# Optimization experiments

Hardware: AMD Instinct MI355X
Metric: run time of the kernel (lower is better)

The kernel has to match this reference:

```python
import jax, jax.numpy as jnp
import numpy as np

INPUT_DIM = 1024
HIDDEN_DIM = 512
SEQ_LEN = 512


def setup_inputs() -> dict:
    key = jax.random.key(0)
    ks = jax.random.split(key, 7)
    s = 1.0 / np.sqrt(INPUT_DIM)
    s2 = 1.0 / np.sqrt(HIDDEN_DIM)
    return {
        "vectors": jax.random.normal(ks[0], (1, SEQ_LEN, INPUT_DIM), dtype=jnp.float32),
        "W_h": jax.random.uniform(ks[1], (HIDDEN_DIM, INPUT_DIM), jnp.float32, -s, s),
        "b_h": jax.random.uniform(ks[2], (HIDDEN_DIM,), jnp.float32, -s, s),
        "W_m": jax.random.uniform(ks[3], (HIDDEN_DIM, INPUT_DIM), jnp.float32, -s, s),
        "b_m": jax.random.uniform(ks[4], (HIDDEN_DIM,), jnp.float32, -s, s),
        "w2": jax.random.uniform(ks[5], (HIDDEN_DIM,), jnp.float32, -s2, s2),
        "b2": jax.random.uniform(ks[6], (), jnp.float32, -s2, s2),
    }


def reference(vectors, W_h, b_h, W_m, b_m, w2, b2):
    # vectors: [1, S, D] -> squeeze leading batch dim (matches torch .squeeze(0))
    x = vectors[0]  # [S, D]
    # Two batched GEMMs replacing the per-token Python loop
    H = x @ W_h.T + b_h  # [S, Hd] head representations
    M = x @ W_m.T + b_m  # [S, Hd] modifier representations
    # Pairwise broadcast add + tanh + dot with layer_2 weights -> [S, S] scores
    pair = jnp.tanh(H[:, None, :] + M[None, :, :])  # [S, S, Hd]
    scores = jnp.einsum('hmd,d->hm', pair, w2) + b2
    return scores
```

## Files before the change

### kernel.cpp

```cpp
#include <hip/hip_runtime.h>

#define C2 2.8853900817779268f
#define DIN 1024
#define HD 512

__device__ __forceinline__ float rcp_fast(float x){ return __builtin_amdgcn_rcpf(x); }
__device__ __forceinline__ float exp2_fast(float x){ return __builtin_amdgcn_exp2f(x); }
__device__ __forceinline__ float comp4(const float4& v, int i){
    return i==0 ? v.x : i==1 ? v.y : i==2 ? v.z : v.w;
}

__global__ __launch_bounds__(256, 4) void gemm_kernel(
    const float* __restrict__ x, const float* __restrict__ Wh,
    const float* __restrict__ Wm, float* __restrict__ P)
{
    int mat = blockIdx.z >> 3, slice = blockIdx.z & 7;
    const float* W = mat ? Wm : Wh;
    int s0 = blockIdx.y * 64, j0 = blockIdx.x * 64;
    int k0base = slice * 128;
    __shared__ float Xs[64 * 32];
    __shared__ float Ws[64 * 32];
    int tid = threadIdx.x;
    int tx = tid & 15, ty = tid >> 4;
    int lrow = tid >> 3, lq = tid & 7;

    const float* xp = x + (size_t)(s0 + lrow) * DIN + k0base + lq * 4;
    const float* wp = W + (size_t)(j0 + lrow) * DIN + k0base + lq * 4;

    auto sidx = [](int row, int q){ return row * 32 + ((q ^ ((row >> 2) & 7)) << 2); };

    float4 xr0, xr1, wr0, wr1;
    auto load_chunk = [&](int c){
        int off = c * 32;
        xr0 = *(const float4*)(xp + off);
        xr1 = *(const float4*)(xp + off + 32 * DIN);
        wr0 = *(const float4*)(wp + off);
        wr1 = *(const float4*)(wp + off + 32 * DIN);
    };
    auto store_chunk = [&](){
        *(float4*)&Xs[sidx(lrow, lq)]      = xr0;
        *(float4*)&Xs[sidx(lrow + 32, lq)] = xr1;
        *(float4*)&Ws[sidx(lrow, lq)]      = wr0;
        *(float4*)&Ws[sidx(lrow + 32, lq)] = wr1;
    };

    float acc[4][4] = {};
    load_chunk(0);
    for (int c = 0; c < 4; c++){
        __syncthreads();
        store_chunk();
        __syncthreads();
        if (c < 3) load_chunk(c + 1);
        #pragma unroll
        for (int qk = 0; qk < 8; qk++){
            float4 a4[4], b4[4];
            #pragma unroll
            for (int i = 0; i < 4; i++)
                a4[i] = *(const float4*)&Xs[(ty*4 + i) * 32 + ((qk ^ (ty & 7)) << 2)];
            #pragma unroll
            for (int j = 0; j < 4; j++)
                b4[j] = *(const float4*)&Ws[(tx*4 + j) * 32 + ((qk ^ (tx & 7)) << 2)];
            #pragma unroll
            for (int i = 0; i < 4; i++)
                #pragma unroll
                for (int j = 0; j < 4; j++){
                    acc[i][j] = fmaf(a4[i].x, b4[j].x, acc[i][j]);
                    acc[i][j] = fmaf(a4[i].y, b4[j].y, acc[i][j]);
                    acc[i][j] = fmaf(a4[i].z, b4[j].z, acc[i][j]);
                    acc[i][j] = fmaf(a4[i].w, b4[j].w, acc[i][j]);
                }
        }
    }
    float* Pp = P + (size_t)(mat * 8 + slice) * 262144;
    #pragma unroll
    for (int i = 0; i < 4; i++){
        int r = s0 + ty * 4 + i;
        float4 v = {acc[i][0], acc[i][1], acc[i][2], acc[i][3]};
        *(float4*)&Pp[r * HD + j0 + tx * 4] = v;
    }
}

__global__ __launch_bounds__(256) void finalize_kernel(
    const float* __restrict__ P, const float* __restrict__ bh,
    const float* __restrict__ bm, float* __restrict__ EH, float* __restrict__ EM)
{
    int g = blockIdx.x * 256 + threadIdx.x;
    int mat = g >> 16;
    int r4 = g & 65535;
    int col4 = r4 & 127;
    const float4* P4 = (const float4*)P + (size_t)mat * 8 * 65536;
    float4 a = P4[r4];
    #pragma unroll
    for (int sl = 1; sl < 8; sl++){
        float4 b = P4[sl * 65536 + r4];
        a.x += b.x; a.y += b.y; a.z += b.z; a.w += b.w;
    }
    float4 bias = ((const float4*)(mat ? bm : bh))[col4];
    float4 e = { exp2_fast(C2 * (a.x + bias.x)), exp2_fast(C2 * (a.y + bias.y)),
                 exp2_fast(C2 * (a.z + bias.z)), exp2_fast(C2 * (a.w + bias.w)) };
    ((float4*)(mat ? EM : EH))[r4] = e;
}

__global__ __launch_bounds__(256, 4) void scores_kernel(
    const float* __restrict__ EH, const float* __restrict__ EM,
    const float* __restrict__ w2, float* __restrict__ Q)
{
    int m0 = blockIdx.x * 64, h0 = blockIdx.y * 32, d0 = blockIdx.z * 64;
    __shared__ float Hs[32 * 68];
    __shared__ float Ms[64 * 68];
    __shared__ float wsS[64];
    int tid = threadIdx.x;
    int tx = tid & 15, ty = tid >> 4;
    #pragma unroll
    for (int l = 0; l < 2; l++){
        int slot = tid + 256 * l;
        int row = slot >> 4, q = slot & 15;
        float4 h = *(const float4*)(EH + (size_t)(h0 + row) * HD + d0 + q * 4);
        *(float4*)&Hs[row * 68 + q * 4] = h;
    }
    #pragma unroll
    for (int l = 0; l < 4; l++){
        int slot = tid + 256 * l;
        int m = slot >> 4, q = slot & 15;
        float4 v = *(const float4*)(EM + (size_t)(m0 + m) * HD + d0 + q * 4);
        Ms[(q*4 + 0) * 68 + m] = v.x;
        Ms[(q*4 + 1) * 68 + m] = v.y;
        Ms[(q*4 + 2) * 68 + m] = v.z;
        Ms[(q*4 + 3) * 68 + m] = v.w;
    }
    if (tid < 16){
        float4 w = *(const float4*)(w2 + d0 + tid * 4);
        float4 ws = {-2.f * w.x, -2.f * w.y, -2.f * w.z, -2.f * w.w};
        *(float4*)&wsS[tid * 4] = ws;
    }
    __syncthreads();

    float acc[2][4] = {};
    #pragma unroll 2
    for (int it = 0; it < 16; it++){
        int dk = it * 4;
        float4 w4 = *(const float4*)&wsS[dk];
        float4 hA = *(const float4*)&Hs[(ty*2 + 0) * 68 + dk];
        float4 hB = *(const float4*)&Hs[(ty*2 + 1) * 68 + dk];
        #pragma unroll
        for (int dd = 0; dd < 4; dd++){
            float4 mv = *(const float4*)&Ms[(dk + dd) * 68 + tx * 4];
            float w = comp4(w4, dd);
            float e0 = comp4(hA, dd), e1 = comp4(hB, dd);
            acc[0][0] = fmaf(w, rcp_fast(fmaf(e0, mv.x, 1.f)), acc[0][0]);
            acc[0][1] = fmaf(w, rcp_fast(fmaf(e0, mv.y, 1.f)), acc[0][1]);
            acc[0][2] = fmaf(w, rcp_fast(fmaf(e0, mv.z, 1.f)), acc[0][2]);
            acc[0][3] = fmaf(w, rcp_fast(fmaf(e0, mv.w, 1.f)), acc[0][3]);
            acc[1][0] = fmaf(w, rcp_fast(fmaf(e1, mv.x, 1.f)), acc[1][0]);
            acc[1][1] = fmaf(w, rcp_fast(fmaf(e1, mv.y, 1.f)), acc[1][1]);
            acc[1][2] = fmaf(w, rcp_fast(fmaf(e1, mv.z, 1.f)), acc[1][2]);
            acc[1][3] = fmaf(w, rcp_fast(fmaf(e1, mv.w, 1.f)), acc[1][3]);
        }
    }
    float* Qp = Q + (size_t)blockIdx.z * 262144;
    #pragma unroll
    for (int i = 0; i < 2; i++){
        float4 v = {acc[i][0], acc[i][1], acc[i][2], acc[i][3]};
        *(float4*)&Qp[(h0 + ty*2 + i) * 512 + m0 + tx * 4] = v;
    }
}

__global__ __launch_bounds__(256) void combine_kernel(
    const float* __restrict__ Q, const float* __restrict__ w2,
    const float* __restrict__ b2, float* __restrict__ out)
{
    int tid = threadIdx.x;
    __shared__ float red[4];
    __shared__ float c0s;
    float s = 0.f;
    if (tid < 128){ float4 v = ((const float4*)w2)[tid]; s = v.x + v.y + v.z + v.w; }
    #pragma unroll
    for (int off = 32; off; off >>= 1) s += __shfl_down(s, off, 64);
    if (tid < 128 && (tid & 63) == 0) red[tid >> 6] = s;
    __syncthreads();
    if (tid == 0) c0s = red[0] + red[1] + b2[0];
    __syncthreads();
    float c0 = c0s;
    int g = blockIdx.x * 256 + tid;
    const float4* Q4 = (const float4*)Q;
    float4 a = Q4[g];
    #pragma unroll
    for (int sl = 1; sl < 8; sl++){
        float4 b = Q4[sl * 65536 + g];
        a.x += b.x; a.y += b.y; a.z += b.z; a.w += b.w;
    }
    float4 o = {a.x + c0, a.y + c0, a.z + c0, a.w + c0};
    ((float4*)out)[g] = o;
}

extern "C" void kernel_launch(void* const* d_in, const int* in_sizes, int n_in,
                              void* d_out, int out_size, void* d_ws, size_t ws_size,
                              hipStream_t stream) {
    const float* x   = (const float*)d_in[0];
    const float* Wh  = (const float*)d_in[1];
    const float* bh  = (const float*)d_in[2];
    const float* Wm  = (const float*)d_in[3];
    const float* bm  = (const float*)d_in[4];
    const float* w2  = (const float*)d_in[5];
    const float* b2  = (const float*)d_in[6];
    float* out = (float*)d_out;
    (void)in_sizes; (void)n_in; (void)out_size; (void)ws_size;

    float* w  = (float*)d_ws;
    float* EH = w;
    float* EM = w + 262144;
    float* P  = w + 524288;
    float* Q  = w + 524288 + 16 * 262144;

    gemm_kernel<<<dim3(8, 8, 16), 256, 0, stream>>>(x, Wh, Wm, P);
    finalize_kernel<<<512, 256, 0, stream>>>(P, bh, bm, EH, EM);
    scores_kernel<<<dim3(8, 16, 8), 256, 0, stream>>>(EH, EM, w2, Q);
    combine_kernel<<<256, 256, 0, stream>>>(Q, w2, b2, out);
}
```

Baseline: 114.3 us.

## Replace FP32 split-K GEMM with bf16 MFMA GEMM fused with exp epilogue

Converts x, W_h and W_m to bf16 in a new pre-pass kernel. A new MFMA 16x16x32 bf16 GEMM then computes the full K reduction per wave and applies the bias plus exp2 epilogue directly. This removes the split-K partial buffer and the separate finalize reduction kernel, and moves the GEMM from FP32 FMA to matrix cores. In exchange it adds a conversion pass over the weights on every call, lowers precision to bf16, and loads MFMA fragments straight from global memory without LDS staging.

```diff
diff --git a/kernel.cpp b/kernel.cpp
--- a/kernel.cpp
+++ b/kernel.cpp
@@ -4,101 +4,65 @@
 #define DIN 1024
 #define HD 512
 
+typedef short short8 __attribute__((ext_vector_type(8)));
+typedef float floatx4 __attribute__((ext_vector_type(4)));
+
 __device__ __forceinline__ float rcp_fast(float x){ return __builtin_amdgcn_rcpf(x); }
 __device__ __forceinline__ float exp2_fast(float x){ return __builtin_amdgcn_exp2f(x); }
 __device__ __forceinline__ float comp4(const float4& v, int i){
     return i==0 ? v.x : i==1 ? v.y : i==2 ? v.z : v.w;
 }
+__device__ __forceinline__ unsigned short f2bf(float f){
+    union{float f; unsigned int u;} v; v.f = f;
+    unsigned int u = v.u;
+    return (unsigned short)((u + 0x7FFFu + ((u >> 16) & 1u)) >> 16);
+}
 
-__global__ __launch_bounds__(256, 4) void gemm_kernel(
+__global__ __launch_bounds__(256) void convert_kernel(
     const float* __restrict__ x, const float* __restrict__ Wh,
-    const float* __restrict__ Wm, float* __restrict__ P)
+    const float* __restrict__ Wm, unsigned short* __restrict__ xb,
+    unsigned short* __restrict__ whb, unsigned short* __restrict__ wmb)
 {
-    int mat = blockIdx.z >> 3, slice = blockIdx.z & 7;
-    const float* W = mat ? Wm : Wh;
-    int s0 = blockIdx.y * 64, j0 = blockIdx.x * 64;
-    int k0base = slice * 128;
-    __shared__ float Xs[64 * 32];
-    __shared__ float Ws[64 * 32];
-    int tid = threadIdx.x;
-    int tx = tid & 15, ty = tid >> 4;
-    int lrow = tid >> 3, lq = tid & 7;
+    int r = blockIdx.z;
+    const float* s = r == 0 ? x : r == 1 ? Wh : Wm;
+    unsigned short* d = r == 0 ? xb : r == 1 ? whb : wmb;
+    int i = (blockIdx.x * 256 + threadIdx.x) * 4;
+    float4 v = *(const float4*)(s + i);
+    ushort4 o = { f2bf(v.x), f2bf(v.y), f2bf(v.z), f2bf(v.w) };
+    *(ushort4*)(d + i) = o;
+}
 
-    const float* xp = x + (size_t)(s0 + lrow) * DIN + k0base + lq * 4;
-    const float* wp = W + (size_t)(j0 + lrow) * DIN + k0base + lq * 4;
+__global__ __launch_bounds__(256) void mfma_gemm_kernel(
+    const unsigned short* __restrict__ xb, const unsigned short* __restrict__ whb,
+    const unsigned short* __restrict__ wmb, const float* __restrict__ bh,
+    const float* __restrict__ bm, float* __restrict__ EH, float* __restrict__ EM)
+{
+    int mat = blockIdx.z;
+    const unsigned short* B = mat ? wmb : whb;
+    const float* bias = mat ? bm : bh;
+    float* O = mat ? EM : EH;
+    int j0 = blockIdx.x * 32, s0 = blockIdx.y * 32;
+    int wave = threadIdx.x >> 6, lane = threadIdx.x & 63;
+    int sw = (wave & 1) * 16, jw = (wave >> 1) * 16;
+    int m = lane & 15, quad = lane >> 4;
 
-    auto sidx = [](int row, int q){ return row * 32 + ((q ^ ((row >> 2) & 7)) << 2); };
+    const unsigned short* ap = xb + (size_t)(s0 + sw + m) * DIN + quad * 8;
+    const unsigned short* bp = B  + (size_t)(j0 + jw + m) * DIN + quad * 8;
 
-    float4 xr0, xr1, wr0, wr1;
-    auto load_chunk = [&](int c){
-        int off = c * 32;
-        xr0 = *(const float4*)(xp + off);
-        xr1 = *(const float4*)(xp + off + 32 * DIN);
-        wr0 = *(const float4*)(wp + off);
-        wr1 = *(const float4*)(wp + off + 32 * DIN);
-    };
-    auto store_chunk = [&](){
-        *(float4*)&Xs[sidx(lrow, lq)]      = xr0;
-        *(float4*)&Xs[sidx(lrow + 32, lq)] = xr1;
-        *(float4*)&Ws[sidx(lrow, lq)]      = wr0;
-        *(float4*)&Ws[sidx(lrow + 32, lq)] = wr1;
-    };
-
-    float acc[4][4] = {};
-    load_chunk(0);
-    for (int c = 0; c < 4; c++){
-        __syncthreads();
-        store_chunk();
-        __syncthreads();
-        if (c < 3) load_chunk(c + 1);
-        #pragma unroll
-        for (int qk = 0; qk < 8; qk++){
-            float4 a4[4], b4[4];
-            #pragma unroll
-            for (int i = 0; i < 4; i++)
-                a4[i] = *(const float4*)&Xs[(ty*4 + i) * 32 + ((qk ^ (ty & 7)) << 2)];
-            #pragma unroll
-            for (int j = 0; j < 4; j++)
-                b4[j] = *(const float4*)&Ws[(tx*4 + j) * 32 + ((qk ^ (tx & 7)) << 2)];
-            #pragma unroll
-            for (int i = 0; i < 4; i++)
-                #pragma unroll
-                for (int j = 0; j < 4; j++){
-                    acc[i][j] = fmaf(a4[i].x, b4[j].x, acc[i][j]);
-                    acc[i][j] = fmaf(a4[i].y, b4[j].y, acc[i][j]);
-                    acc[i][j] = fmaf(a4[i].z, b4[j].z, acc[i][j]);
-                    acc[i][j] = fmaf(a4[i].w, b4[j].w, acc[i][j]);
-                }
-        }
+    floatx4 acc = {0.f, 0.f, 0.f, 0.f};
+    #pragma unroll 8
+    for (int k = 0; k < DIN; k += 32){
+        short8 af = *(const short8*)(ap + k);
+        short8 bf = *(const short8*)(bp + k);
+        acc = __builtin_amdgcn_mfma_f32_16x16x32_bf16(af, bf, acc, 0, 0, 0);
     }
-    float* Pp = P + (size_t)(mat * 8 + slice) * 262144;
+    int col = j0 + jw + m;
+    float bv = bias[col];
     #pragma unroll
     for (int i = 0; i < 4; i++){
-        int r = s0 + ty * 4 + i;
-        float4 v = {acc[i][0], acc[i][1], acc[i][2], acc[i][3]};
-        *(float4*)&Pp[r * HD + j0 + tx * 4] = v;
+        int row = s0 + sw + quad * 4 + i;
+        O[(size_t)row * HD + col] = exp2_fast(C2 * (acc[i] + bv));
     }
-}
-
-__global__ __launch_bounds__(256) void finalize_kernel(
-    const float* __restrict__ P, const float* __restrict__ bh,
-    const float* __restrict__ bm, float* __restrict__ EH, float* __restrict__ EM)
-{
-    int g = blockIdx.x * 256 + threadIdx.x;
-    int mat = g >> 16;
-    int r4 = g & 65535;
-    int col4 = r4 & 127;
-    const float4* P4 = (const float4*)P + (size_t)mat * 8 * 65536;
-    float4 a = P4[r4];
-    #pragma unroll
-    for (int sl = 1; sl < 8; sl++){
-        float4 b = P4[sl * 65536 + r4];
-        a.x += b.x; a.y += b.y; a.z += b.z; a.w += b.w;
-    }
-    float4 bias = ((const float4*)(mat ? bm : bh))[col4];
-    float4 e = { exp2_fast(C2 * (a.x + bias.x)), exp2_fast(C2 * (a.y + bias.y)),
-                 exp2_fast(C2 * (a.z + bias.z)), exp2_fast(C2 * (a.w + bias.w)) };
-    ((float4*)(mat ? EM : EH))[r4] = e;
 }
 
 __global__ __launch_bounds__(256, 4) void scores_kernel(
@@ -121,12 +85,12 @@
     #pragma unroll
     for (int l = 0; l < 4; l++){
         int slot = tid + 256 * l;
-        int m = slot >> 4, q = slot & 15;
-        float4 v = *(const float4*)(EM + (size_t)(m0 + m) * HD + d0 + q * 4);
-        Ms[(q*4 + 0) * 68 + m] = v.x;
-        Ms[(q*4 + 1) * 68 + m] = v.y;
-        Ms[(q*4 + 2) * 68 + m] = v.z;
-        Ms[(q*4 + 3) * 68 + m] = v.w;
+        int mm = slot >> 4, q = slot & 15;
+        float4 v = *(const float4*)(EM + (size_t)(m0 + mm) * HD + d0 + q * 4);
+        Ms[(q*4 + 0) * 68 + mm] = v.x;
+        Ms[(q*4 + 1) * 68 + mm] = v.y;
+        Ms[(q*4 + 2) * 68 + mm] = v.z;
+        Ms[(q*4 + 3) * 68 + mm] = v.w;
     }
     if (tid < 16){
         float4 w = *(const float4*)(w2 + d0 + tid * 4);
@@ -206,14 +170,16 @@
     float* out = (float*)d_out;
     (void)in_sizes; (void)n_in; (void)out_size; (void)ws_size;
 
-    float* w  = (float*)d_ws;
-    float* EH = w;
-    float* EM = w + 262144;
-    float* P  = w + 524288;
-    float* Q  = w + 524288 + 16 * 262144;
+    float* w = (float*)d_ws;
+    unsigned short* xb  = (unsigned short*)(w);
+    unsigned short* whb = (unsigned short*)(w + 262144);
+    unsigned short* wmb = (unsigned short*)(w + 524288);
+    float* EH = w + 786432;
+    float* EM = w + 1048576;
+    float* Q  = w + 1310720;
 
-    gemm_kernel<<<dim3(8, 8, 16), 256, 0, stream>>>(x, Wh, Wm, P);
-    finalize_kernel<<<512, 256, 0, stream>>>(P, bh, bm, EH, EM);
+    convert_kernel<<<dim3(512, 1, 3), 256, 0, stream>>>(x, Wh, Wm, xb, whb, wmb);
+    mfma_gemm_kernel<<<dim3(16, 16, 2), 256, 0, stream>>>(xb, whb, wmb, bh, bm, EH, EM);
     scores_kernel<<<dim3(8, 16, 8), 256, 0, stream>>>(EH, EM, w2, Q);
     combine_kernel<<<256, 256, 0, stream>>>(Q, w2, b2, out);
 }
```

After: 109.2 us (median of 2 runs). 4.5% less time.
